# Kernel optimization log

Measured on AMD Instinct MI355X. Metric: run time of the kernel, lower is better.

Reference implementation:

```python
import jax, jax.numpy as jnp
import numpy as np

A = 10      # n_trained_players = n_trained_off(5) + n_trained_def(5)
T = 65      # timesteps; scan runs T-1 = 64 steps
B = 128     # batch
XD, YD, ZD, HD, MD, RM = 2, 20, 64, 256, 90, 256
LOG2PI = float(np.log(2.0 * np.pi))


def _lin(x, W, b):
    # batched per-agent linear: x [A,B,in], W [A,in,out], b [A,out]
    return jnp.einsum('abi,aio->abo', x, W) + b[:, None, :]


def _mlp2(x, W1, b1, W2, b2):
    return jax.nn.relu(_lin(jax.nn.relu(_lin(x, W1, b1)), W2, b2))


def setup_inputs() -> dict:
    key = jax.random.key(0)
    ks = jax.random.split(key, 40)
    s = 0.05
    def w(i, shape):
        return jax.random.normal(ks[i], shape, dtype=jnp.float32) * s
    enc_in, pri_in, dec_in, gru_in = XD + MD + RM, MD + RM, YD + MD + ZD + RM, XD + ZD
    inp = {
        'data': jax.random.normal(ks[0], (T, B, YD), dtype=jnp.float32),
        'macro': jax.random.randint(ks[1], (T, B, A), 0, MD),
        'eps': jax.random.normal(ks[2], (T - 1, A, B, ZD), dtype=jnp.float32),
        'enc_W1': w(3, (A, enc_in, HD)), 'enc_b1': w(4, (A, HD)),
        'enc_W2': w(5, (A, HD, HD)), 'enc_b2': w(6, (A, HD)),
        'encm_W': w(7, (A, HD, ZD)), 'encm_b': w(8, (A, ZD)),
        'encs_W': w(9, (A, HD, ZD)), 'encs_b': w(10, (A, ZD)),
        'pri_W1': w(11, (A, pri_in, HD)), 'pri_b1': w(12, (A, HD)),
        'pri_W2': w(13, (A, HD, HD)), 'pri_b2': w(14, (A, HD)),
        'prim_W': w(15, (A, HD, ZD)), 'prim_b': w(16, (A, ZD)),
        'pris_W': w(17, (A, HD, ZD)), 'pris_b': w(18, (A, ZD)),
        'dec_W1': w(19, (A, dec_in, HD)), 'dec_b1': w(20, (A, HD)),
        'dec_W2': w(21, (A, HD, HD)), 'dec_b2': w(22, (A, HD)),
        'decm_W': w(23, (A, HD, XD)), 'decm_b': w(24, (A, XD)),
        'decs_W': w(25, (A, HD, XD)), 'decs_b': w(26, (A, XD)),
        'gru_Wih': w(27, (A, gru_in, 3 * RM)), 'gru_bih': w(28, (A, 3 * RM)),
        'gru_Whh': w(29, (A, RM, 3 * RM)), 'gru_bhh': w(30, (A, 3 * RM)),
    }
    return inp


def _forward(data, macro, eps, enc_W1, enc_b1, enc_W2, enc_b2, encm_W, encm_b,
             encs_W, encs_b, pri_W1, pri_b1, pri_W2, pri_b2, prim_W, prim_b,
             pris_W, pris_b, dec_W1, dec_b1, dec_W2, dec_b2, decm_W, decm_b,
             decs_W, decs_b, gru_Wih, gru_bih, gru_Whh, gru_bhh):
    # x: next-step per-player positions [T-1, A, B, 2]
    x = data[1:].reshape(T - 1, B, A, XD).transpose(0, 2, 1, 3)
    # macro one-hot, [T, A, B, 90]
    m = jax.nn.one_hot(macro, MD, dtype=data.dtype).transpose(0, 2, 1, 3)
    h0 = jnp.zeros((A, B, RM), data.dtype)
    zero = jnp.zeros((), data.dtype)

    def step(carry, ts):
        h, recon, kl = carry
        x_t, y_t, m_t, e_t = ts  # [A,B,2], [B,20], [A,B,90], [A,B,ZD]
        yb = jnp.broadcast_to(y_t[None], (A, B, YD))
        # encoder q(z|x,m,h)
        enc_h = _mlp2(jnp.concatenate([x_t, m_t, h], -1), enc_W1, enc_b1, enc_W2, enc_b2)
        enc_mean = _lin(enc_h, encm_W, encm_b)
        enc_std = jax.nn.softplus(_lin(enc_h, encs_W, encs_b))
        # prior p(z|m,h)
        pri_h = _mlp2(jnp.concatenate([m_t, h], -1), pri_W1, pri_b1, pri_W2, pri_b2)
        pri_mean = _lin(pri_h, prim_W, prim_b)
        pri_std = jax.nn.softplus(_lin(pri_h, pris_W, pris_b))
        # reparameterized sample
        z_t = enc_mean + e_t * enc_std
        # decoder p(x|y,m,z,h)
        dec_h = _mlp2(jnp.concatenate([yb, m_t, z_t, h], -1), dec_W1, dec_b1, dec_W2, dec_b2)
        dec_mean = _lin(dec_h, decm_W, decm_b)
        dec_std = jax.nn.softplus(_lin(dec_h, decs_W, decs_b))
        # per-agent 1-layer GRU (torch gate order: reset, update, new)
        gi = _lin(jnp.concatenate([x_t, z_t], -1), gru_Wih, gru_bih)
        gh = _lin(h, gru_Whh, gru_bhh)
        ir, iz, inn = jnp.split(gi, 3, axis=-1)
        hr, hz, hn = jnp.split(gh, 3, axis=-1)
        r = jax.nn.sigmoid(ir + hr)
        u = jax.nn.sigmoid(iz + hz)
        n = jnp.tanh(inn + r * hn)
        h_new = (1.0 - u) * n + u * h
        # losses (summed over all agents/batch/dims, as in torch code)
        kl = kl + 0.5 * jnp.sum(2.0 * jnp.log(pri_std) - 2.0 * jnp.log(enc_std)
                                + (enc_std ** 2 + (enc_mean - pri_mean) ** 2) / pri_std ** 2 - 1.0)
        recon = recon + jnp.sum(0.5 * ((x_t - dec_mean) / dec_std) ** 2
                                + jnp.log(dec_std) + 0.5 * LOG2PI)
        return (h_new, recon, kl), None

    xs = (x, data[:-1], m[:-1], eps)
    (_, recon, kl), _ = jax.lax.scan(step, (h0, zero, zero), xs)
    return recon, kl


def reference(data, macro, eps, enc_W1, enc_b1, enc_W2, enc_b2, encm_W, encm_b,
              encs_W, encs_b, pri_W1, pri_b1, pri_W2, pri_b2, prim_W, prim_b,
              pris_W, pris_b, dec_W1, dec_b1, dec_W2, dec_b2, decm_W, decm_b,
              decs_W, decs_b, gru_Wih, gru_bih, gru_Whh, gru_bhh):
    return _forward(data, macro, eps, enc_W1, enc_b1, enc_W2, enc_b2, encm_W, encm_b,
                    encs_W, encs_b, pri_W1, pri_b1, pri_W2, pri_b2, prim_W, prim_b,
                    pris_W, pris_b, dec_W1, dec_b1, dec_W2, dec_b2, decm_W, decm_b,
                    decs_W, decs_b, gru_Wih, gru_bih, gru_Whh, gru_bhh)
```

## Files before the change

kernel.cpp:

```cpp
#include <hip/hip_runtime.h>
#include <math.h>

#define NA 10
#define NT 65
#define NB 128
#define XDIM 2
#define YDIM 20
#define ZDIM 64
#define HDIM 256
#define RMDIM 256
#define NSTEP 64
#define TS 8
#define HR (TS + 1)
#define LOG2PI 1.8378770664093453f

#define ENC_W1_S (348 * 256)
#define PRI_W1_S (346 * 256)
#define DEC_W1_S (430 * 256)
#define GRU_WIH_S (66 * 768)
#define GRU_WHH_S (256 * 768)
#define W2_S (256 * 256)
#define HEADW_S (256 * 64)
#define SZH (NA * NB * 256)
#define SZZ (NA * NB * ZDIM)

static __device__ __forceinline__ float sp(float x) {
    return fmaxf(x, 0.f) + log1pf(expf(-fabsf(x)));
}
static __device__ __forceinline__ float sigm(float x) { return 1.f / (1.f + expf(-x)); }
static __device__ __forceinline__ float relu(float x) { return fmaxf(x, 0.f); }

__device__ __forceinline__ void chunk_fma8(float acc[8], const float4* Xs4, int m,
                                           const float* __restrict__ W, int wld, int n0u) {
#pragma unroll 4
    for (int kk4 = 0; kk4 < 16; ++kk4) {
        float4 xv = Xs4[m * 16 + (kk4 ^ (m & 15))];
        const float* w0 = W + (kk4 * 4) * wld + n0u;
        const float* w1 = w0 + wld;
        const float* w2 = w1 + wld;
        const float* w3 = w2 + wld;
#pragma unroll
        for (int j = 0; j < 8; ++j) acc[j] = fmaf(xv.x, w0[j], acc[j]);
#pragma unroll
        for (int j = 0; j < 8; ++j) acc[j] = fmaf(xv.y, w1[j], acc[j]);
#pragma unroll
        for (int j = 0; j < 8; ++j) acc[j] = fmaf(xv.z, w2[j], acc[j]);
#pragma unroll
        for (int j = 0; j < 8; ++j) acc[j] = fmaf(xv.w, w3[j], acc[j]);
    }
}

__device__ __forceinline__ void stage64(float4* Xs4, int tid, const float* __restrict__ src,
                                        int ld) {
    int tr = tid >> 4, tc = tid & 15;
#pragma unroll
    for (int p = 0; p < 4; ++p) {
        int row = tr + p * 16;
        float4 v = *(const float4*)(src + row * ld + tc * 4);
        Xs4[row * 16 + (tc ^ (row & 15))] = v;
    }
}

__device__ __forceinline__ void stage64_pad(float4* Xs4, int tid, const float* __restrict__ src,
                                            int ld, int ncols) {
    int tr = tid >> 4, tc = tid & 15;
#pragma unroll
    for (int p = 0; p < 4; ++p) {
        int row = tr + p * 16;
        float4 v = make_float4(0.f, 0.f, 0.f, 0.f);
        if (tc * 4 < ncols) v = *(const float4*)(src + row * ld + tc * 4);
        Xs4[row * 16 + (tc ^ (row & 15))] = v;
    }
}

__device__ __forceinline__ void store_tile32(float* Sf, int tid, const float vals[8],
                                             float* __restrict__ outbase, int oldim) {
    int lane = tid & 63, wv = tid >> 6;
    __syncthreads();
#pragma unroll
    for (int j = 0; j < 8; ++j) Sf[lane * 36 + wv * 8 + j] = vals[j];
    __syncthreads();
    int r = tid >> 2, q = tid & 3;
    float4 v0 = *(float4*)(Sf + r * 36 + q * 8);
    float4 v1 = *(float4*)(Sf + r * 36 + q * 8 + 4);
    *(float4*)(outbase + r * oldim + q * 8) = v0;
    *(float4*)(outbase + r * oldim + q * 8 + 4) = v1;
}

__global__ __launch_bounds__(256) void k_init(float* __restrict__ h0, double* __restrict__ accd) {
    int i = blockIdx.x * 256 + threadIdx.x;
    ((float4*)h0)[i] = make_float4(0.f, 0.f, 0.f, 0.f);
    if (i == 0) {
        accd[0] = 0.0;
        accd[1] = 0.0;
    }
}

__global__ __launch_bounds__(256) void kS1(const float* __restrict__ h,
                                           const float* __restrict__ enc_W1,
                                           const float* __restrict__ enc_b1,
                                           const float* __restrict__ pri_W1,
                                           const float* __restrict__ pri_b1,
                                           const float* __restrict__ gru_Whh,
                                           const float* __restrict__ gru_bhh,
                                           const float* __restrict__ data,
                                           const int* __restrict__ macro, float* __restrict__ ench1,
                                           float* __restrict__ prih1, float* __restrict__ ghB,
                                           int t) {
    __shared__ float4 Xs4[64 * 16];
    int tid = threadIdx.x, bid = blockIdx.x;
    int lane = tid & 63, wv = tid >> 6;
    int ep, a, b0, c0;
    const float* Wb;
    int wld;
    float* outp;
    int oldim;
    if (bid < 160) {
        ep = 0; a = bid / 16; int r = bid % 16; b0 = (r >> 3) * 64; c0 = (r & 7) * 32;
        Wb = enc_W1 + a * ENC_W1_S + 92 * 256; wld = 256; outp = ench1; oldim = 256;
    } else if (bid < 320) {
        int q = bid - 160;
        ep = 1; a = q / 16; int r = q % 16; b0 = (r >> 3) * 64; c0 = (r & 7) * 32;
        Wb = pri_W1 + a * PRI_W1_S + 90 * 256; wld = 256; outp = prih1; oldim = 256;
    } else {
        int q = bid - 320;
        ep = 2; a = q / 48; int r = q % 48; b0 = (r >= 24) ? 64 : 0; c0 = (r % 24) * 32;
        Wb = gru_Whh + a * GRU_WHH_S; wld = 768; outp = ghB; oldim = 768;
    }
    int n0u = __builtin_amdgcn_readfirstlane(c0 + wv * 8);
    const float* X = h + (a * NB + b0) * RMDIM;
    float acc[8] = {};
    for (int kb = 0; kb < 256; kb += 64) {
        stage64(Xs4, tid, X + kb, RMDIM);
        __syncthreads();
        chunk_fma8(acc, Xs4, lane, Wb + kb * wld, wld, n0u);
        __syncthreads();
    }
    float vals[8];
    int row = b0 + lane;
    if (ep == 2) {
#pragma unroll
        for (int j = 0; j < 8; ++j) vals[j] = acc[j] + gru_bhh[a * 768 + n0u + j];
    } else {
        const float* W1b = (ep == 0) ? enc_W1 + a * ENC_W1_S : pri_W1 + a * PRI_W1_S;
        const float* bb = (ep == 0) ? enc_b1 + a * HDIM : pri_b1 + a * HDIM;
        int mi = macro[(t * NB + row) * NA + a];
        const float* mrow = W1b + (ep == 0 ? 2 + mi : mi) * 256;
        float xv0 = 0.f, xv1 = 0.f;
        if (ep == 0) {
            xv0 = data[(t + 1) * (NB * YDIM) + row * YDIM + a * XDIM];
            xv1 = data[(t + 1) * (NB * YDIM) + row * YDIM + a * XDIM + 1];
        }
#pragma unroll
        for (int j = 0; j < 8; ++j) {
            float v = acc[j] + bb[n0u + j] + mrow[n0u + j];
            if (ep == 0) v += xv0 * W1b[n0u + j] + xv1 * W1b[256 + n0u + j];
            vals[j] = relu(v);
        }
    }
    store_tile32((float*)Xs4, tid, vals, outp + (a * NB + b0) * oldim + c0, oldim);
}

__global__ __launch_bounds__(256) void kS2(const float* __restrict__ ench1,
                                           const float* __restrict__ prih1,
                                           const float* __restrict__ enc_W2,
                                           const float* __restrict__ enc_b2,
                                           const float* __restrict__ pri_W2,
                                           const float* __restrict__ pri_b2,
                                           float* __restrict__ ench2, float* __restrict__ prih2) {
    __shared__ float4 Xs4[64 * 16];
    int tid = threadIdx.x, bid = blockIdx.x;
    int lane = tid & 63, wv = tid >> 6;
    int isenc = bid < 160;
    int q = isenc ? bid : bid - 160;
    int a = q / 16;
    int r = q % 16;
    int b0 = (r >> 3) * 64, c0 = (r & 7) * 32;
    int n0u = __builtin_amdgcn_readfirstlane(c0 + wv * 8);
    const float* X = (isenc ? ench1 : prih1) + (a * NB + b0) * HDIM;
    const float* Wb = (isenc ? enc_W2 : pri_W2) + a * W2_S;
    const float* bb = (isenc ? enc_b2 : pri_b2) + a * HDIM;
    float acc[8] = {};
    for (int kb = 0; kb < 256; kb += 64) {
        stage64(Xs4, tid, X + kb, HDIM);
        __syncthreads();
        chunk_fma8(acc, Xs4, lane, Wb + kb * 256, 256, n0u);
        __syncthreads();
    }
    float vals[8];
#pragma unroll
    for (int j = 0; j < 8; ++j) vals[j] = relu(acc[j] + bb[n0u + j]);
    float* outp = isenc ? ench2 : prih2;
    store_tile32((float*)Xs4, tid, vals, outp + (a * NB + b0) * HDIM + c0, HDIM);
}

__global__ __launch_bounds__(256) void kS3(const float* __restrict__ ench2,
                                           const float* __restrict__ prih2,
                                           const float* __restrict__ encm_W,
                                           const float* __restrict__ encm_b,
                                           const float* __restrict__ encs_W,
                                           const float* __restrict__ encs_b,
                                           const float* __restrict__ prim_W,
                                           const float* __restrict__ prim_b,
                                           const float* __restrict__ pris_W,
                                           const float* __restrict__ pris_b,
                                           float* __restrict__ heads) {
    __shared__ float4 Xs4[64 * 16];
    int tid = threadIdx.x, bid = blockIdx.x;
    int lane = tid & 63, wv = tid >> 6;
    int a = bid / 16;
    int r = bid % 16;
    int b0 = (r >> 3) * 64;
    int hc = r & 7;
    int head = hc >> 1, c0 = (hc & 1) * 32;
    const float* Wt;
    const float* Bt;
    if (head == 0) { Wt = encm_W; Bt = encm_b; }
    else if (head == 1) { Wt = encs_W; Bt = encs_b; }
    else if (head == 2) { Wt = prim_W; Bt = prim_b; }
    else { Wt = pris_W; Bt = pris_b; }
    int n0u = __builtin_amdgcn_readfirstlane(c0 + wv * 8);
    const float* X = (head < 2 ? ench2 : prih2) + (a * NB + b0) * HDIM;
    const float* Wb = Wt + a * HEADW_S;
    float acc[8] = {};
    for (int kb = 0; kb < 256; kb += 64) {
        stage64(Xs4, tid, X + kb, HDIM);
        __syncthreads();
        chunk_fma8(acc, Xs4, lane, Wb + kb * ZDIM, ZDIM, n0u);
        __syncthreads();
    }
    float vals[8];
#pragma unroll
    for (int j = 0; j < 8; ++j) vals[j] = acc[j] + Bt[a * ZDIM + n0u + j];
    store_tile32((float*)Xs4, tid, vals, heads + (a * NB + b0) * 256 + head * 64 + c0, 256);
}

__global__ __launch_bounds__(256) void kS4(const float* __restrict__ heads,
                                           const float* __restrict__ eps,
                                           const float* __restrict__ data,
                                           const float* __restrict__ gru_Wih,
                                           const float* __restrict__ gru_bih,
                                           const float* __restrict__ ghB,
                                           const float* __restrict__ h_t, float* __restrict__ h_nx,
                                           float* __restrict__ z_t, double* __restrict__ accd,
                                           int t) {
    __shared__ float4 Xs4[64 * 16];
    __shared__ float red[256];
    int tid = threadIdx.x, bid = blockIdx.x;
    int lane = tid & 63, wv = tid >> 6;
    int a = bid / 16;
    int r = bid % 16;
    int b0 = (r >> 3) * 64, c0 = (r & 7) * 32;
    int n0u = __builtin_amdgcn_readfirstlane(c0 + wv * 8);
    {
        int tr = tid >> 4, tc = tid & 15;
#pragma unroll
        for (int p = 0; p < 4; ++p) {
            int rw = tr + p * 16;
            const float* hh = heads + (a * NB + b0 + rw) * 256 + tc * 4;
            float4 em = *(const float4*)hh;
            float4 es = *(const float4*)(hh + 64);
            const float* ee = eps + ((t * NA + a) * NB + b0 + rw) * ZDIM + tc * 4;
            float4 ev = *(const float4*)ee;
            float4 zv;
            zv.x = em.x + ev.x * sp(es.x);
            zv.y = em.y + ev.y * sp(es.y);
            zv.z = em.z + ev.z * sp(es.z);
            zv.w = em.w + ev.w * sp(es.w);
            Xs4[rw * 16 + (tc ^ (rw & 15))] = zv;
            if (c0 == 0) *(float4*)(z_t + (a * NB + b0 + rw) * ZDIM + tc * 4) = zv;
        }
    }
    __syncthreads();
    float acc[3][8] = {};
    const float* Wihz = gru_Wih + a * GRU_WIH_S + 2 * 768;
#pragma unroll
    for (int g = 0; g < 3; ++g) chunk_fma8(acc[g], Xs4, lane, Wihz, 768, g * 256 + n0u);
    int row = b0 + lane;
    float xv0 = data[(t + 1) * (NB * YDIM) + row * YDIM + a * XDIM];
    float xv1 = data[(t + 1) * (NB * YDIM) + row * YDIM + a * XDIM + 1];
    const float* Wih0 = gru_Wih + a * GRU_WIH_S;
    const float* bih = gru_bih + a * 768;
    const float* ghr = ghB + (a * NB + row) * 768;
    const float* hor = h_t + (a * NB + row) * 256;
    float vals[8];
#pragma unroll
    for (int j = 0; j < 8; ++j) {
        int cr = n0u + j;
        float gi0 = acc[0][j] + bih[cr] + xv0 * Wih0[cr] + xv1 * Wih0[768 + cr];
        float gi1 = acc[1][j] + bih[256 + cr] + xv0 * Wih0[256 + cr] + xv1 * Wih0[768 + 256 + cr];
        float gi2 = acc[2][j] + bih[512 + cr] + xv0 * Wih0[512 + cr] + xv1 * Wih0[768 + 512 + cr];
        float hrv = ghr[cr], hzv = ghr[256 + cr], hnv = ghr[512 + cr];
        float hov = hor[cr];
        float rr = sigm(gi0 + hrv);
        float uu = sigm(gi1 + hzv);
        float nn = tanhf(gi2 + rr * hnv);
        vals[j] = (1.f - uu) * nn + uu * hov;
    }
    store_tile32((float*)Xs4, tid, vals, h_nx + (a * NB + b0) * 256 + c0, 256);
    if (c0 == 0) {
        float part = 0.f;
        for (int qq = tid; qq < 1024; qq += 256) {
            int rw = qq >> 4, z4 = (qq & 15) * 4;
            const float* hh = heads + (a * NB + b0 + rw) * 256 + z4;
            float4 em = *(const float4*)hh;
            float4 es4 = *(const float4*)(hh + 64);
            float4 pm = *(const float4*)(hh + 128);
            float4 ps4 = *(const float4*)(hh + 192);
#pragma unroll
            for (int e = 0; e < 4; ++e) {
                float emv = (&em.x)[e], esv = sp((&es4.x)[e]);
                float pmv = (&pm.x)[e], psv = sp((&ps4.x)[e]);
                float dm = emv - pmv;
                part += 0.5f * (2.f * logf(psv) - 2.f * logf(esv) +
                                (esv * esv + dm * dm) / (psv * psv) - 1.f);
            }
        }
        red[tid] = part;
        __syncthreads();
#pragma unroll
        for (int s = 128; s > 0; s >>= 1) {
            if (tid < s) red[tid] += red[tid + s];
            __syncthreads();
        }
        if (tid == 0) atomicAdd(&accd[1], (double)red[0]);
    }
}

__global__ __launch_bounds__(256) void kDec1(const float* __restrict__ data,
                                             const int* __restrict__ macro,
                                             const float* __restrict__ z_ring,
                                             const float* __restrict__ h_ring,
                                             const float* __restrict__ dec_W1,
                                             const float* __restrict__ dec_b1,
                                             float* __restrict__ dech1s, int t0) {
    __shared__ float4 Xs4[64 * 16];
    int tid = threadIdx.x, bid = blockIdx.x;
    int lane = tid & 63, wv = tid >> 6;
    int ti = bid / 160;
    int rem = bid % 160;
    int a = rem / 16;
    int r = rem % 16;
    int b0 = (r >> 3) * 64, c0 = (r & 7) * 32;
    int t = t0 + ti;
    int n0u = __builtin_amdgcn_readfirstlane(c0 + wv * 8);
    const float* Wb = dec_W1 + a * DEC_W1_S;
    float acc[8] = {};
    stage64_pad(Xs4, tid, data + t * (NB * YDIM) + b0 * YDIM, YDIM, 20);
    __syncthreads();
    chunk_fma8(acc, Xs4, lane, Wb, 256, n0u);
    __syncthreads();
    stage64(Xs4, tid, z_ring + (size_t)(t % TS) * SZZ + (a * NB + b0) * ZDIM, ZDIM);
    __syncthreads();
    chunk_fma8(acc, Xs4, lane, Wb + 110 * 256, 256, n0u);
    __syncthreads();
    const float* X = h_ring + (size_t)(t % HR) * SZH + (a * NB + b0) * 256;
    for (int kb = 0; kb < 256; kb += 64) {
        stage64(Xs4, tid, X + kb, 256);
        __syncthreads();
        chunk_fma8(acc, Xs4, lane, Wb + (174 + kb) * 256, 256, n0u);
        __syncthreads();
    }
    int row = b0 + lane;
    int mi = macro[(t * NB + row) * NA + a];
    const float* mrow = Wb + (20 + mi) * 256;
    const float* bb = dec_b1 + a * HDIM;
    float vals[8];
#pragma unroll
    for (int j = 0; j < 8; ++j) vals[j] = relu(acc[j] + bb[n0u + j] + mrow[n0u + j]);
    store_tile32((float*)Xs4, tid, vals, dech1s + ((ti * NA + a) * NB + b0) * 256 + c0, 256);
}

__global__ __launch_bounds__(256) void kDec2(const float* __restrict__ dech1s,
                                             const float* __restrict__ dec_W2,
                                             const float* __restrict__ dec_b2,
                                             float* __restrict__ dech2s) {
    __shared__ float4 Xs4[64 * 16];
    int tid = threadIdx.x, bid = blockIdx.x;
    int lane = tid & 63, wv = tid >> 6;
    int ti = bid / 160;
    int rem = bid % 160;
    int a = rem / 16;
    int r = rem % 16;
    int b0 = (r >> 3) * 64, c0 = (r & 7) * 32;
    int n0u = __builtin_amdgcn_readfirstlane(c0 + wv * 8);
    const float* X = dech1s + ((ti * NA + a) * NB + b0) * 256;
    const float* Wb = dec_W2 + a * W2_S;
    float acc[8] = {};
    for (int kb = 0; kb < 256; kb += 64) {
        stage64(Xs4, tid, X + kb, 256);
        __syncthreads();
        chunk_fma8(acc, Xs4, lane, Wb + kb * 256, 256, n0u);
        __syncthreads();
    }
    const float* bb = dec_b2 + a * HDIM;
    float vals[8];
#pragma unroll
    for (int j = 0; j < 8; ++j) vals[j] = relu(acc[j] + bb[n0u + j]);
    store_tile32((float*)Xs4, tid, vals, dech2s + ((ti * NA + a) * NB + b0) * 256 + c0, 256);
}

__global__ __launch_bounds__(256) void kEpi(const float* __restrict__ dech2s,
                                            const float* __restrict__ decm_W,
                                            const float* __restrict__ decm_b,
                                            const float* __restrict__ decs_W,
                                            const float* __restrict__ decs_b,
                                            const float* __restrict__ data,
                                            double* __restrict__ accd, int t0) {
    int tid = threadIdx.x;
    int widx = blockIdx.x * 4 + (tid >> 6);
    int lane = tid & 63;
    int ti = widx / 1280;
    int rem = widx - ti * 1280;
    int a = rem >> 7, b = rem & 127;
    int targ = t0 + ti + 1;
    const float4 hv = *(const float4*)&dech2s[((ti * NA + a) * NB + b) * HDIM + lane * 4];
    const float* wmb = decm_W + a * (HDIM * XDIM) + lane * 8;
    const float4 wm0 = *(const float4*)&wmb[0];
    const float4 wm1 = *(const float4*)&wmb[4];
    const float* wsb = decs_W + a * (HDIM * XDIM) + lane * 8;
    const float4 ws0 = *(const float4*)&wsb[0];
    const float4 ws1 = *(const float4*)&wsb[4];
    float m0 = hv.x * wm0.x + hv.y * wm0.z + hv.z * wm1.x + hv.w * wm1.z;
    float m1 = hv.x * wm0.y + hv.y * wm0.w + hv.z * wm1.y + hv.w * wm1.w;
    float s0 = hv.x * ws0.x + hv.y * ws0.z + hv.z * ws1.x + hv.w * ws1.z;
    float s1 = hv.x * ws0.y + hv.y * ws0.w + hv.z * ws1.y + hv.w * ws1.w;
#pragma unroll
    for (int off = 32; off > 0; off >>= 1) {
        m0 += __shfl_down(m0, off, 64);
        m1 += __shfl_down(m1, off, 64);
        s0 += __shfl_down(s0, off, 64);
        s1 += __shfl_down(s1, off, 64);
    }
    if (lane == 0) {
        float dm0 = m0 + decm_b[a * 2 + 0];
        float dm1 = m1 + decm_b[a * 2 + 1];
        float ds0 = sp(s0 + decs_b[a * 2 + 0]);
        float ds1 = sp(s1 + decs_b[a * 2 + 1]);
        float x0 = data[targ * (NB * YDIM) + b * YDIM + a * XDIM + 0];
        float x1 = data[targ * (NB * YDIM) + b * YDIM + a * XDIM + 1];
        float r0 = (x0 - dm0) / ds0, r1 = (x1 - dm1) / ds1;
        float tt = 0.5f * r0 * r0 + logf(ds0) + 0.5f * LOG2PI + 0.5f * r1 * r1 + logf(ds1) +
                   0.5f * LOG2PI;
        atomicAdd(&accd[0], (double)tt);
    }
}

__global__ void k_final(const double* __restrict__ accd, float* __restrict__ out) {
    if (threadIdx.x == 0) {
        out[0] = (float)accd[0];
        out[1] = (float)accd[1];
    }
}

extern "C" void kernel_launch(void* const* d_in, const int* in_sizes, int n_in, void* d_out,
                              int out_size, void* d_ws, size_t ws_size, hipStream_t stream) {
    const float* data = (const float*)d_in[0];
    const int* macro = (const int*)d_in[1];
    const float* eps = (const float*)d_in[2];
    const float* enc_W1 = (const float*)d_in[3];
    const float* enc_b1 = (const float*)d_in[4];
    const float* enc_W2 = (const float*)d_in[5];
    const float* enc_b2 = (const float*)d_in[6];
    const float* encm_W = (const float*)d_in[7];
    const float* encm_b = (const float*)d_in[8];
    const float* encs_W = (const float*)d_in[9];
    const float* encs_b = (const float*)d_in[10];
    const float* pri_W1 = (const float*)d_in[11];
    const float* pri_b1 = (const float*)d_in[12];
    const float* pri_W2 = (const float*)d_in[13];
    const float* pri_b2 = (const float*)d_in[14];
    const float* prim_W = (const float*)d_in[15];
    const float* prim_b = (const float*)d_in[16];
    const float* pris_W = (const float*)d_in[17];
    const float* pris_b = (const float*)d_in[18];
    const float* dec_W1 = (const float*)d_in[19];
    const float* dec_b1 = (const float*)d_in[20];
    const float* dec_W2 = (const float*)d_in[21];
    const float* dec_b2 = (const float*)d_in[22];
    const float* decm_W = (const float*)d_in[23];
    const float* decm_b = (const float*)d_in[24];
    const float* decs_W = (const float*)d_in[25];
    const float* decs_b = (const float*)d_in[26];
    const float* gru_Wih = (const float*)d_in[27];
    const float* gru_bih = (const float*)d_in[28];
    const float* gru_Whh = (const float*)d_in[29];
    const float* gru_bhh = (const float*)d_in[30];

    double* accd = (double*)d_ws;
    float* base = (float*)((char*)d_ws + 256);
    float* h_ring = base;
    float* z_ring = h_ring + (size_t)HR * SZH;
    float* ench1 = z_ring + (size_t)TS * SZZ;
    float* prih1 = ench1 + SZH;
    float* ench2 = prih1 + SZH;
    float* prih2 = ench2 + SZH;
    float* heads = prih2 + SZH;
    float* ghB = heads + SZH;
    float* dech1s = ghB + NA * NB * 768;
    float* dech2s = dech1s + (size_t)TS * SZH;
    float* out = (float*)d_out;

    k_init<<<320, 256, 0, stream>>>(h_ring, accd);
    for (int t = 0; t < NSTEP; ++t) {
        float* h_t = h_ring + (size_t)(t % HR) * SZH;
        float* h_nx = h_ring + (size_t)((t + 1) % HR) * SZH;
        float* z_t = z_ring + (size_t)(t % TS) * SZZ;
        kS1<<<800, 256, 0, stream>>>(h_t, enc_W1, enc_b1, pri_W1, pri_b1, gru_Whh, gru_bhh, data,
                                     macro, ench1, prih1, ghB, t);
        kS2<<<320, 256, 0, stream>>>(ench1, prih1, enc_W2, enc_b2, pri_W2, pri_b2, ench2, prih2);
        kS3<<<160, 256, 0, stream>>>(ench2, prih2, encm_W, encm_b, encs_W, encs_b, prim_W, prim_b,
                                     pris_W, pris_b, heads);
        kS4<<<160, 256, 0, stream>>>(heads, eps, data, gru_Wih, gru_bih, ghB, h_t, h_nx, z_t, accd,
                                     t);
        if ((t % TS) == TS - 1) {
            int t0 = t - TS + 1;
            kDec1<<<TS * 160, 256, 0, stream>>>(data, macro, z_ring, h_ring, dec_W1, dec_b1,
                                                dech1s, t0);
            kDec2<<<TS * 160, 256, 0, stream>>>(dech1s, dec_W2, dec_b2, dech2s);
            kEpi<<<TS * 320, 256, 0, stream>>>(dech2s, decm_W, decm_b, decs_W, decs_b, data, accd,
                                               t0);
        }
    }
    k_final<<<1, 64, 0, stream>>>(accd, out);
}
```

Before: 10.35 ms.

## Switch activations to feature-major layout, drop LDS staging, fuse heads with reparam/KL

All hidden-state buffers are stored transposed as [agent][feature][batch]. Each thread can then read its own batch row directly from global memory with coalesced loads, so the LDS staging, swizzle and the store_tile32 shuffle go away. The head kernel now computes the reparameterised z and the KL term itself, which removes the intermediate heads buffer and the KL pass inside kS4. The cost is that the GEMM inner loops read X straight from global or L2 with no shared reuse across waves. kEpi now makes strided scalar loads instead of float4 loads.

```diff
diff --git a/kernel.cpp b/kernel.cpp
--- a/kernel.cpp
+++ b/kernel.cpp
@@ -21,71 +21,16 @@
 #define GRU_WHH_S (256 * 768)
 #define W2_S (256 * 256)
 #define HEADW_S (256 * 64)
-#define SZH (NA * NB * 256)
-#define SZZ (NA * NB * ZDIM)
+
+#define SA (256 * NB)
+#define GA (768 * NB)
+#define ZA (ZDIM * NB)
 
 static __device__ __forceinline__ float sp(float x) {
     return fmaxf(x, 0.f) + log1pf(expf(-fabsf(x)));
 }
 static __device__ __forceinline__ float sigm(float x) { return 1.f / (1.f + expf(-x)); }
 static __device__ __forceinline__ float relu(float x) { return fmaxf(x, 0.f); }
-
-__device__ __forceinline__ void chunk_fma8(float acc[8], const float4* Xs4, int m,
-                                           const float* __restrict__ W, int wld, int n0u) {
-#pragma unroll 4
-    for (int kk4 = 0; kk4 < 16; ++kk4) {
-        float4 xv = Xs4[m * 16 + (kk4 ^ (m & 15))];
-        const float* w0 = W + (kk4 * 4) * wld + n0u;
-        const float* w1 = w0 + wld;
-        const float* w2 = w1 + wld;
-        const float* w3 = w2 + wld;
-#pragma unroll
-        for (int j = 0; j < 8; ++j) acc[j] = fmaf(xv.x, w0[j], acc[j]);
-#pragma unroll
-        for (int j = 0; j < 8; ++j) acc[j] = fmaf(xv.y, w1[j], acc[j]);
-#pragma unroll
-        for (int j = 0; j < 8; ++j) acc[j] = fmaf(xv.z, w2[j], acc[j]);
-#pragma unroll
-        for (int j = 0; j < 8; ++j) acc[j] = fmaf(xv.w, w3[j], acc[j]);
-    }
-}
-
-__device__ __forceinline__ void stage64(float4* Xs4, int tid, const float* __restrict__ src,
-                                        int ld) {
-    int tr = tid >> 4, tc = tid & 15;
-#pragma unroll
-    for (int p = 0; p < 4; ++p) {
-        int row = tr + p * 16;
-        float4 v = *(const float4*)(src + row * ld + tc * 4);
-        Xs4[row * 16 + (tc ^ (row & 15))] = v;
-    }
-}
-
-__device__ __forceinline__ void stage64_pad(float4* Xs4, int tid, const float* __restrict__ src,
-                                            int ld, int ncols) {
-    int tr = tid >> 4, tc = tid & 15;
-#pragma unroll
-    for (int p = 0; p < 4; ++p) {
-        int row = tr + p * 16;
-        float4 v = make_float4(0.f, 0.f, 0.f, 0.f);
-        if (tc * 4 < ncols) v = *(const float4*)(src + row * ld + tc * 4);
-        Xs4[row * 16 + (tc ^ (row & 15))] = v;
-    }
-}
-
-__device__ __forceinline__ void store_tile32(float* Sf, int tid, const float vals[8],
-                                             float* __restrict__ outbase, int oldim) {
-    int lane = tid & 63, wv = tid >> 6;
-    __syncthreads();
-#pragma unroll
-    for (int j = 0; j < 8; ++j) Sf[lane * 36 + wv * 8 + j] = vals[j];
-    __syncthreads();
-    int r = tid >> 2, q = tid & 3;
-    float4 v0 = *(float4*)(Sf + r * 36 + q * 8);
-    float4 v1 = *(float4*)(Sf + r * 36 + q * 8 + 4);
-    *(float4*)(outbase + r * oldim + q * 8) = v0;
-    *(float4*)(outbase + r * oldim + q * 8 + 4) = v1;
-}
 
 __global__ __launch_bounds__(256) void k_init(float* __restrict__ h0, double* __restrict__ accd) {
     int i = blockIdx.x * 256 + threadIdx.x;
@@ -107,40 +52,43 @@
                                            const int* __restrict__ macro, float* __restrict__ ench1,
                                            float* __restrict__ prih1, float* __restrict__ ghB,
                                            int t) {
-    __shared__ float4 Xs4[64 * 16];
-    int tid = threadIdx.x, bid = blockIdx.x;
-    int lane = tid & 63, wv = tid >> 6;
-    int ep, a, b0, c0;
+    int tid = threadIdx.x, bid = blockIdx.x;
+    int lane = tid & 63, wv = tid >> 6;
+    int a = bid / 80;
+    int r = bid % 80;
+    int b0 = (r & 1) * 64;
+    int tile = r >> 1;
+    int ep, c0;
     const float* Wb;
     int wld;
-    float* outp;
-    int oldim;
-    if (bid < 160) {
-        ep = 0; a = bid / 16; int r = bid % 16; b0 = (r >> 3) * 64; c0 = (r & 7) * 32;
-        Wb = enc_W1 + a * ENC_W1_S + 92 * 256; wld = 256; outp = ench1; oldim = 256;
-    } else if (bid < 320) {
-        int q = bid - 160;
-        ep = 1; a = q / 16; int r = q % 16; b0 = (r >> 3) * 64; c0 = (r & 7) * 32;
-        Wb = pri_W1 + a * PRI_W1_S + 90 * 256; wld = 256; outp = prih1; oldim = 256;
+    if (tile < 8) {
+        ep = 0; c0 = tile * 32;
+        Wb = enc_W1 + a * ENC_W1_S + 92 * 256; wld = 256;
+    } else if (tile < 16) {
+        ep = 1; c0 = (tile - 8) * 32;
+        Wb = pri_W1 + a * PRI_W1_S + 90 * 256; wld = 256;
     } else {
-        int q = bid - 320;
-        ep = 2; a = q / 48; int r = q % 48; b0 = (r >= 24) ? 64 : 0; c0 = (r % 24) * 32;
-        Wb = gru_Whh + a * GRU_WHH_S; wld = 768; outp = ghB; oldim = 768;
+        ep = 2; c0 = (tile - 16) * 32;
+        Wb = gru_Whh + a * GRU_WHH_S; wld = 768;
     }
     int n0u = __builtin_amdgcn_readfirstlane(c0 + wv * 8);
-    const float* X = h + (a * NB + b0) * RMDIM;
+    int row = b0 + lane;
+    const float* X = h + a * SA + row;
+    const float* wp = Wb + n0u;
     float acc[8] = {};
-    for (int kb = 0; kb < 256; kb += 64) {
-        stage64(Xs4, tid, X + kb, RMDIM);
-        __syncthreads();
-        chunk_fma8(acc, Xs4, lane, Wb + kb * wld, wld, n0u);
-        __syncthreads();
-    }
-    float vals[8];
-    int row = b0 + lane;
+#pragma unroll 8
+    for (int k = 0; k < 256; ++k) {
+        float xv = X[k * NB];
+        const float* wr = wp + k * wld;
+#pragma unroll
+        for (int j = 0; j < 8; ++j) acc[j] = fmaf(xv, wr[j], acc[j]);
+    }
     if (ep == 2) {
 #pragma unroll
-        for (int j = 0; j < 8; ++j) vals[j] = acc[j] + gru_bhh[a * 768 + n0u + j];
+        for (int j = 0; j < 8; ++j) {
+            float v = acc[j] + gru_bhh[a * 768 + n0u + j];
+            ghB[a * GA + (n0u + j) * NB + row] = v;
+        }
     } else {
         const float* W1b = (ep == 0) ? enc_W1 + a * ENC_W1_S : pri_W1 + a * PRI_W1_S;
         const float* bb = (ep == 0) ? enc_b1 + a * HDIM : pri_b1 + a * HDIM;
@@ -151,14 +99,14 @@
             xv0 = data[(t + 1) * (NB * YDIM) + row * YDIM + a * XDIM];
             xv1 = data[(t + 1) * (NB * YDIM) + row * YDIM + a * XDIM + 1];
         }
+        float* outp = (ep == 0) ? ench1 : prih1;
 #pragma unroll
         for (int j = 0; j < 8; ++j) {
             float v = acc[j] + bb[n0u + j] + mrow[n0u + j];
             if (ep == 0) v += xv0 * W1b[n0u + j] + xv1 * W1b[256 + n0u + j];
-            vals[j] = relu(v);
+            outp[a * SA + (n0u + j) * NB + row] = relu(v);
         }
     }
-    store_tile32((float*)Xs4, tid, vals, outp + (a * NB + b0) * oldim + c0, oldim);
 }
 
 __global__ __launch_bounds__(256) void kS2(const float* __restrict__ ench1,
@@ -168,30 +116,31 @@
                                            const float* __restrict__ pri_W2,
                                            const float* __restrict__ pri_b2,
                                            float* __restrict__ ench2, float* __restrict__ prih2) {
-    __shared__ float4 Xs4[64 * 16];
-    int tid = threadIdx.x, bid = blockIdx.x;
-    int lane = tid & 63, wv = tid >> 6;
-    int isenc = bid < 160;
-    int q = isenc ? bid : bid - 160;
-    int a = q / 16;
-    int r = q % 16;
-    int b0 = (r >> 3) * 64, c0 = (r & 7) * 32;
+    int tid = threadIdx.x, bid = blockIdx.x;
+    int lane = tid & 63, wv = tid >> 6;
+    int a = bid / 32;
+    int r = bid % 32;
+    int isenc = (r < 16);
+    int q = isenc ? r : r - 16;
+    int b0 = (q & 1) * 64;
+    int c0 = (q >> 1) * 32;
     int n0u = __builtin_amdgcn_readfirstlane(c0 + wv * 8);
-    const float* X = (isenc ? ench1 : prih1) + (a * NB + b0) * HDIM;
-    const float* Wb = (isenc ? enc_W2 : pri_W2) + a * W2_S;
+    int row = b0 + lane;
+    const float* X = (isenc ? ench1 : prih1) + a * SA + row;
+    const float* wp = (isenc ? enc_W2 : pri_W2) + a * W2_S + n0u;
     const float* bb = (isenc ? enc_b2 : pri_b2) + a * HDIM;
     float acc[8] = {};
-    for (int kb = 0; kb < 256; kb += 64) {
-        stage64(Xs4, tid, X + kb, HDIM);
-        __syncthreads();
-        chunk_fma8(acc, Xs4, lane, Wb + kb * 256, 256, n0u);
-        __syncthreads();
-    }
-    float vals[8];
-#pragma unroll
-    for (int j = 0; j < 8; ++j) vals[j] = relu(acc[j] + bb[n0u + j]);
+#pragma unroll 8
+    for (int k = 0; k < 256; ++k) {
+        float xv = X[k * NB];
+        const float* wr = wp + k * 256;
+#pragma unroll
+        for (int j = 0; j < 8; ++j) acc[j] = fmaf(xv, wr[j], acc[j]);
+    }
     float* outp = isenc ? ench2 : prih2;
-    store_tile32((float*)Xs4, tid, vals, outp + (a * NB + b0) * HDIM + c0, HDIM);
+#pragma unroll
+    for (int j = 0; j < 8; ++j)
+        outp[a * SA + (n0u + j) * NB + row] = relu(acc[j] + bb[n0u + j]);
 }
 
 __global__ __launch_bounds__(256) void kS3(const float* __restrict__ ench2,
@@ -204,126 +153,109 @@
                                            const float* __restrict__ prim_b,
                                            const float* __restrict__ pris_W,
                                            const float* __restrict__ pris_b,
-                                           float* __restrict__ heads) {
-    __shared__ float4 Xs4[64 * 16];
-    int tid = threadIdx.x, bid = blockIdx.x;
-    int lane = tid & 63, wv = tid >> 6;
-    int a = bid / 16;
-    int r = bid % 16;
-    int b0 = (r >> 3) * 64;
-    int hc = r & 7;
-    int head = hc >> 1, c0 = (hc & 1) * 32;
+                                           const float* __restrict__ eps, float* __restrict__ z_t,
+                                           double* __restrict__ accd, int t) {
+    __shared__ float L[4][16][64];
+    __shared__ float red[256];
+    int tid = threadIdx.x, bid = blockIdx.x;
+    int lane = tid & 63, wv = tid >> 6;
+    int a = bid / 8;
+    int r = bid % 8;
+    int b0 = (r & 1) * 64;
+    int zc0 = (r >> 1) * 16;
+    int row = b0 + lane;
     const float* Wt;
     const float* Bt;
-    if (head == 0) { Wt = encm_W; Bt = encm_b; }
-    else if (head == 1) { Wt = encs_W; Bt = encs_b; }
-    else if (head == 2) { Wt = prim_W; Bt = prim_b; }
+    if (wv == 0) { Wt = encm_W; Bt = encm_b; }
+    else if (wv == 1) { Wt = encs_W; Bt = encs_b; }
+    else if (wv == 2) { Wt = prim_W; Bt = prim_b; }
     else { Wt = pris_W; Bt = pris_b; }
-    int n0u = __builtin_amdgcn_readfirstlane(c0 + wv * 8);
-    const float* X = (head < 2 ? ench2 : prih2) + (a * NB + b0) * HDIM;
-    const float* Wb = Wt + a * HEADW_S;
-    float acc[8] = {};
-    for (int kb = 0; kb < 256; kb += 64) {
-        stage64(Xs4, tid, X + kb, HDIM);
+    const float* X = (wv < 2 ? ench2 : prih2) + a * SA + row;
+    const float* wp = Wt + a * HEADW_S + zc0;
+    float acc[16] = {};
+#pragma unroll 4
+    for (int k = 0; k < 256; ++k) {
+        float xv = X[k * NB];
+        const float* wr = wp + k * ZDIM;
+#pragma unroll
+        for (int j = 0; j < 16; ++j) acc[j] = fmaf(xv, wr[j], acc[j]);
+    }
+#pragma unroll
+    for (int j = 0; j < 16; ++j) L[wv][j][lane] = acc[j] + Bt[a * ZDIM + zc0 + j];
+    __syncthreads();
+    float part = 0.f;
+#pragma unroll
+    for (int q = 0; q < 4; ++q) {
+        int zc = wv * 4 + q;
+        float em = L[0][zc][lane];
+        float es = sp(L[1][zc][lane]);
+        float pm = L[2][zc][lane];
+        float ps = sp(L[3][zc][lane]);
+        float ev = eps[((t * NA + a) * NB + row) * ZDIM + zc0 + zc];
+        z_t[a * ZA + (zc0 + zc) * NB + row] = em + ev * es;
+        float dm = em - pm;
+        part += 0.5f * (2.f * logf(ps) - 2.f * logf(es) + (es * es + dm * dm) / (ps * ps) - 1.f);
+    }
+    red[tid] = part;
+    __syncthreads();
+#pragma unroll
+    for (int s = 128; s > 0; s >>= 1) {
+        if (tid < s) red[tid] += red[tid + s];
         __syncthreads();
-        chunk_fma8(acc, Xs4, lane, Wb + kb * ZDIM, ZDIM, n0u);
-        __syncthreads();
-    }
-    float vals[8];
-#pragma unroll
-    for (int j = 0; j < 8; ++j) vals[j] = acc[j] + Bt[a * ZDIM + n0u + j];
-    store_tile32((float*)Xs4, tid, vals, heads + (a * NB + b0) * 256 + head * 64 + c0, 256);
-}
-
-__global__ __launch_bounds__(256) void kS4(const float* __restrict__ heads,
-                                           const float* __restrict__ eps,
+    }
+    if (tid == 0) atomicAdd(&accd[1], (double)red[0]);
+}
+
+__global__ __launch_bounds__(256) void kS4(const float* __restrict__ z_t,
                                            const float* __restrict__ data,
                                            const float* __restrict__ gru_Wih,
                                            const float* __restrict__ gru_bih,
                                            const float* __restrict__ ghB,
                                            const float* __restrict__ h_t, float* __restrict__ h_nx,
-                                           float* __restrict__ z_t, double* __restrict__ accd,
                                            int t) {
-    __shared__ float4 Xs4[64 * 16];
-    __shared__ float red[256];
     int tid = threadIdx.x, bid = blockIdx.x;
     int lane = tid & 63, wv = tid >> 6;
     int a = bid / 16;
     int r = bid % 16;
-    int b0 = (r >> 3) * 64, c0 = (r & 7) * 32;
+    int b0 = (r & 1) * 64;
+    int c0 = (r >> 1) * 32;
     int n0u = __builtin_amdgcn_readfirstlane(c0 + wv * 8);
-    {
-        int tr = tid >> 4, tc = tid & 15;
-#pragma unroll
-        for (int p = 0; p < 4; ++p) {
-            int rw = tr + p * 16;
-            const float* hh = heads + (a * NB + b0 + rw) * 256 + tc * 4;
-            float4 em = *(const float4*)hh;
-            float4 es = *(const float4*)(hh + 64);
-            const float* ee = eps + ((t * NA + a) * NB + b0 + rw) * ZDIM + tc * 4;
-            float4 ev = *(const float4*)ee;
-            float4 zv;
-            zv.x = em.x + ev.x * sp(es.x);
-            zv.y = em.y + ev.y * sp(es.y);
-            zv.z = em.z + ev.z * sp(es.z);
-            zv.w = em.w + ev.w * sp(es.w);
-            Xs4[rw * 16 + (tc ^ (rw & 15))] = zv;
-            if (c0 == 0) *(float4*)(z_t + (a * NB + b0 + rw) * ZDIM + tc * 4) = zv;
-        }
-    }
-    __syncthreads();
+    int row = b0 + lane;
+    const float* X = z_t + a * ZA + row;
+    const float* wp = gru_Wih + a * GRU_WIH_S + 2 * 768 + n0u;
     float acc[3][8] = {};
-    const float* Wihz = gru_Wih + a * GRU_WIH_S + 2 * 768;
-#pragma unroll
-    for (int g = 0; g < 3; ++g) chunk_fma8(acc[g], Xs4, lane, Wihz, 768, g * 256 + n0u);
-    int row = b0 + lane;
+#pragma unroll 8
+    for (int k = 0; k < 64; ++k) {
+        float xv = X[k * NB];
+        const float* wr = wp + k * 768;
+#pragma unroll
+        for (int j = 0; j < 8; ++j) acc[0][j] = fmaf(xv, wr[j], acc[0][j]);
+#pragma unroll
+        for (int j = 0; j < 8; ++j) acc[1][j] = fmaf(xv, wr[256 + j], acc[1][j]);
+#pragma unroll
+        for (int j = 0; j < 8; ++j) acc[2][j] = fmaf(xv, wr[512 + j], acc[2][j]);
+    }
     float xv0 = data[(t + 1) * (NB * YDIM) + row * YDIM + a * XDIM];
     float xv1 = data[(t + 1) * (NB * YDIM) + row * YDIM + a * XDIM + 1];
     const float* Wih0 = gru_Wih + a * GRU_WIH_S;
     const float* bih = gru_bih + a * 768;
-    const float* ghr = ghB + (a * NB + row) * 768;
-    const float* hor = h_t + (a * NB + row) * 256;
-    float vals[8];
+    const float* ghb = ghB + a * GA + row;
+    const float* hb = h_t + a * SA + row;
+    float* ob = h_nx + a * SA + row;
 #pragma unroll
     for (int j = 0; j < 8; ++j) {
         int cr = n0u + j;
         float gi0 = acc[0][j] + bih[cr] + xv0 * Wih0[cr] + xv1 * Wih0[768 + cr];
         float gi1 = acc[1][j] + bih[256 + cr] + xv0 * Wih0[256 + cr] + xv1 * Wih0[768 + 256 + cr];
         float gi2 = acc[2][j] + bih[512 + cr] + xv0 * Wih0[512 + cr] + xv1 * Wih0[768 + 512 + cr];
-        float hrv = ghr[cr], hzv = ghr[256 + cr], hnv = ghr[512 + cr];
-        float hov = hor[cr];
+        float hrv = ghb[cr * NB];
+        float hzv = ghb[(256 + cr) * NB];
+        float hnv = ghb[(512 + cr) * NB];
+        float hov = hb[cr * NB];
         float rr = sigm(gi0 + hrv);
         float uu = sigm(gi1 + hzv);
         float nn = tanhf(gi2 + rr * hnv);
-        vals[j] = (1.f - uu) * nn + uu * hov;
-    }
-    store_tile32((float*)Xs4, tid, vals, h_nx + (a * NB + b0) * 256 + c0, 256);
-    if (c0 == 0) {
-        float part = 0.f;
-        for (int qq = tid; qq < 1024; qq += 256) {
-            int rw = qq >> 4, z4 = (qq & 15) * 4;
-            const float* hh = heads + (a * NB + b0 + rw) * 256 + z4;
-            float4 em = *(const float4*)hh;
-            float4 es4 = *(const float4*)(hh + 64);
-            float4 pm = *(const float4*)(hh + 128);
-            float4 ps4 = *(const float4*)(hh + 192);
-#pragma unroll
-            for (int e = 0; e < 4; ++e) {
-                float emv = (&em.x)[e], esv = sp((&es4.x)[e]);
-                float pmv = (&pm.x)[e], psv = sp((&ps4.x)[e]);
-                float dm = emv - pmv;
-                part += 0.5f * (2.f * logf(psv) - 2.f * logf(esv) +
-                                (esv * esv + dm * dm) / (psv * psv) - 1.f);
-            }
-        }
-        red[tid] = part;
-        __syncthreads();
-#pragma unroll
-        for (int s = 128; s > 0; s >>= 1) {
-            if (tid < s) red[tid] += red[tid + s];
-            __syncthreads();
-        }
-        if (tid == 0) atomicAdd(&accd[1], (double)red[0]);
+        ob[cr * NB] = (1.f - uu) * nn + uu * hov;
     }
 }
 
@@ -334,70 +266,82 @@
                                              const float* __restrict__ dec_W1,
                                              const float* __restrict__ dec_b1,
                                              float* __restrict__ dech1s, int t0) {
-    __shared__ float4 Xs4[64 * 16];
     int tid = threadIdx.x, bid = blockIdx.x;
     int lane = tid & 63, wv = tid >> 6;
     int ti = bid / 160;
     int rem = bid % 160;
     int a = rem / 16;
     int r = rem % 16;
-    int b0 = (r >> 3) * 64, c0 = (r & 7) * 32;
+    int b0 = (r & 1) * 64;
+    int c0 = (r >> 1) * 32;
     int t = t0 + ti;
     int n0u = __builtin_amdgcn_readfirstlane(c0 + wv * 8);
+    int row = b0 + lane;
     const float* Wb = dec_W1 + a * DEC_W1_S;
+    const float* wp = Wb + n0u;
     float acc[8] = {};
-    stage64_pad(Xs4, tid, data + t * (NB * YDIM) + b0 * YDIM, YDIM, 20);
-    __syncthreads();
-    chunk_fma8(acc, Xs4, lane, Wb, 256, n0u);
-    __syncthreads();
-    stage64(Xs4, tid, z_ring + (size_t)(t % TS) * SZZ + (a * NB + b0) * ZDIM, ZDIM);
-    __syncthreads();
-    chunk_fma8(acc, Xs4, lane, Wb + 110 * 256, 256, n0u);
-    __syncthreads();
-    const float* X = h_ring + (size_t)(t % HR) * SZH + (a * NB + b0) * 256;
-    for (int kb = 0; kb < 256; kb += 64) {
-        stage64(Xs4, tid, X + kb, 256);
-        __syncthreads();
-        chunk_fma8(acc, Xs4, lane, Wb + (174 + kb) * 256, 256, n0u);
-        __syncthreads();
-    }
-    int row = b0 + lane;
+    const float* yrow = data + t * (NB * YDIM) + row * YDIM;
+#pragma unroll 4
+    for (int k = 0; k < YDIM; ++k) {
+        float xv = yrow[k];
+        const float* wr = wp + k * 256;
+#pragma unroll
+        for (int j = 0; j < 8; ++j) acc[j] = fmaf(xv, wr[j], acc[j]);
+    }
+    const float* Xz = z_ring + (size_t)(t % TS) * (NA * ZA) + a * ZA + row;
+#pragma unroll 8
+    for (int k = 0; k < ZDIM; ++k) {
+        float xv = Xz[k * NB];
+        const float* wr = wp + (110 + k) * 256;
+#pragma unroll
+        for (int j = 0; j < 8; ++j) acc[j] = fmaf(xv, wr[j], acc[j]);
+    }
+    const float* Xh = h_ring + (size_t)(t % HR) * (NA * SA) + a * SA + row;
+#pragma unroll 8
+    for (int k = 0; k < 256; ++k) {
+        float xv = Xh[k * NB];
+        const float* wr = wp + (174 + k) * 256;
+#pragma unroll
+        for (int j = 0; j < 8; ++j) acc[j] = fmaf(xv, wr[j], acc[j]);
+    }
     int mi = macro[(t * NB + row) * NA + a];
     const float* mrow = Wb + (20 + mi) * 256;
     const float* bb = dec_b1 + a * HDIM;
-    float vals[8];
-#pragma unroll
-    for (int j = 0; j < 8; ++j) vals[j] = relu(acc[j] + bb[n0u + j] + mrow[n0u + j]);
-    store_tile32((float*)Xs4, tid, vals, dech1s + ((ti * NA + a) * NB + b0) * 256 + c0, 256);
+    float* ob = dech1s + (size_t)(ti * NA + a) * SA + row;
+#pragma unroll
+    for (int j = 0; j < 8; ++j)
+        ob[(n0u + j) * NB] = relu(acc[j] + bb[n0u + j] + mrow[n0u + j]);
 }
 
 __global__ __launch_bounds__(256) void kDec2(const float* __restrict__ dech1s,
                                              const float* __restrict__ dec_W2,
                                              const float* __restrict__ dec_b2,
                                              float* __restrict__ dech2s) {
-    __shared__ float4 Xs4[64 * 16];
     int tid = threadIdx.x, bid = blockIdx.x;
     int lane = tid & 63, wv = tid >> 6;
     int ti = bid / 160;
     int rem = bid % 160;
     int a = rem / 16;
     int r = rem % 16;
-    int b0 = (r >> 3) * 64, c0 = (r & 7) * 32;
+    int b0 = (r & 1) * 64;
+    int c0 = (r >> 1) * 32;
     int n0u = __builtin_amdgcn_readfirstlane(c0 + wv * 8);
-    const float* X = dech1s + ((ti * NA + a) * NB + b0) * 256;
-    const float* Wb = dec_W2 + a * W2_S;
+    int row = b0 + lane;
+    const float* X = dech1s + (size_t)(ti * NA + a) * SA + row;
+    const float* wp = dec_W2 + a * W2_S + n0u;
+    const float* bb = dec_b2 + a * HDIM;
     float acc[8] = {};
-    for (int kb = 0; kb < 256; kb += 64) {
-        stage64(Xs4, tid, X + kb, 256);
-        __syncthreads();
-        chunk_fma8(acc, Xs4, lane, Wb + kb * 256, 256, n0u);
-        __syncthreads();
-    }
-    const float* bb = dec_b2 + a * HDIM;
-    float vals[8];
-#pragma unroll
-    for (int j = 0; j < 8; ++j) vals[j] = relu(acc[j] + bb[n0u + j]);
-    store_tile32((float*)Xs4, tid, vals, dech2s + ((ti * NA + a) * NB + b0) * 256 + c0, 256);
+#pragma unroll 8
+    for (int k = 0; k < 256; ++k) {
+        float xv = X[k * NB];
+        const float* wr = wp + k * 256;
+#pragma unroll
+        for (int j = 0; j < 8; ++j) acc[j] = fmaf(xv, wr[j], acc[j]);
+    }
+    float* ob = dech2s + (size_t)(ti * NA + a) * SA + row;
+#pragma unroll
+    for (int j = 0; j < 8; ++j)
+        ob[(n0u + j) * NB] = relu(acc[j] + bb[n0u + j]);
 }
 
 __global__ __launch_bounds__(256) void kEpi(const float* __restrict__ dech2s,
@@ -414,17 +358,21 @@
     int rem = widx - ti * 1280;
     int a = rem >> 7, b = rem & 127;
     int targ = t0 + ti + 1;
-    const float4 hv = *(const float4*)&dech2s[((ti * NA + a) * NB + b) * HDIM + lane * 4];
+    const float* dbase = dech2s + (size_t)(ti * NA + a) * SA + b;
+    float hv0 = dbase[(lane * 4 + 0) * NB];
+    float hv1 = dbase[(lane * 4 + 1) * NB];
+    float hv2 = dbase[(lane * 4 + 2) * NB];
+    float hv3 = dbase[(lane * 4 + 3) * NB];
     const float* wmb = decm_W + a * (HDIM * XDIM) + lane * 8;
     const float4 wm0 = *(const float4*)&wmb[0];
     const float4 wm1 = *(const float4*)&wmb[4];
     const float* wsb = decs_W + a * (HDIM * XDIM) + lane * 8;
     const float4 ws0 = *(const float4*)&wsb[0];
     const float4 ws1 = *(const float4*)&wsb[4];
-    float m0 = hv.x * wm0.x + hv.y * wm0.z + hv.z * wm1.x + hv.w * wm1.z;
-    float m1 = hv.x * wm0.y + hv.y * wm0.w + hv.z * wm1.y + hv.w * wm1.w;
-    float s0 = hv.x * ws0.x + hv.y * ws0.z + hv.z * ws1.x + hv.w * ws1.z;
-    float s1 = hv.x * ws0.y + hv.y * ws0.w + hv.z * ws1.y + hv.w * ws1.w;
+    float m0 = hv0 * wm0.x + hv1 * wm0.z + hv2 * wm1.x + hv3 * wm1.z;
+    float m1 = hv0 * wm0.y + hv1 * wm0.w + hv2 * wm1.y + hv3 * wm1.w;
+    float s0 = hv0 * ws0.x + hv1 * ws0.z + hv2 * ws1.x + hv3 * ws1.z;
+    float s1 = hv0 * ws0.y + hv1 * ws0.w + hv2 * ws1.y + hv3 * ws1.w;
 #pragma unroll
     for (int off = 32; off > 0; off >>= 1) {
         m0 += __shfl_down(m0, off, 64);
@@ -490,29 +438,27 @@
     double* accd = (double*)d_ws;
     float* base = (float*)((char*)d_ws + 256);
     float* h_ring = base;
-    float* z_ring = h_ring + (size_t)HR * SZH;
-    float* ench1 = z_ring + (size_t)TS * SZZ;
-    float* prih1 = ench1 + SZH;
-    float* ench2 = prih1 + SZH;
-    float* prih2 = ench2 + SZH;
-    float* heads = prih2 + SZH;
-    float* ghB = heads + SZH;
-    float* dech1s = ghB + NA * NB * 768;
-    float* dech2s = dech1s + (size_t)TS * SZH;
+    float* z_ring = h_ring + (size_t)HR * NA * SA;
+    float* ench1 = z_ring + (size_t)TS * NA * ZA;
+    float* prih1 = ench1 + NA * SA;
+    float* ench2 = prih1 + NA * SA;
+    float* prih2 = ench2 + NA * SA;
+    float* ghB = prih2 + NA * SA;
+    float* dech1s = ghB + NA * GA;
+    float* dech2s = dech1s + (size_t)TS * NA * SA;
     float* out = (float*)d_out;
 
     k_init<<<320, 256, 0, stream>>>(h_ring, accd);
     for (int t = 0; t < NSTEP; ++t) {
-        float* h_t = h_ring + (size_t)(t % HR) * SZH;
-        float* h_nx = h_ring + (size_t)((t + 1) % HR) * SZH;
-        float* z_t = z_ring + (size_t)(t % TS) * SZZ;
+        float* h_t = h_ring + (size_t)(t % HR) * NA * SA;
+        float* h_nx = h_ring + (size_t)((t + 1) % HR) * NA * SA;
+        float* z_t = z_ring + (size_t)(t % TS) * NA * ZA;
         kS1<<<800, 256, 0, stream>>>(h_t, enc_W1, enc_b1, pri_W1, pri_b1, gru_Whh, gru_bhh, data,
                                      macro, ench1, prih1, ghB, t);
         kS2<<<320, 256, 0, stream>>>(ench1, prih1, enc_W2, enc_b2, pri_W2, pri_b2, ench2, prih2);
-        kS3<<<160, 256, 0, stream>>>(ench2, prih2, encm_W, encm_b, encs_W, encs_b, prim_W, prim_b,
-                                     pris_W, pris_b, heads);
-        kS4<<<160, 256, 0, stream>>>(heads, eps, data, gru_Wih, gru_bih, ghB, h_t, h_nx, z_t, accd,
-                                     t);
+        kS3<<<80, 256, 0, stream>>>(ench2, prih2, encm_W, encm_b, encs_W, encs_b, prim_W, prim_b,
+                                    pris_W, pris_b, eps, z_t, accd, t);
+        kS4<<<160, 256, 0, stream>>>(z_t, data, gru_Wih, gru_bih, ghB, h_t, h_nx, t);
         if ((t % TS) == TS - 1) {
             int t0 = t - TS + 1;
             kDec1<<<TS * 160, 256, 0, stream>>>(data, macro, z_ring, h_ring, dec_W1, dec_b1,
```

Measured after the change: 11.29 ms. +9.1%, slower.
